# Performance work log

Hardware: AMD Instinct MI355X
Metric: run time of the kernel (lower is better)

The kernel has to match this reference:

```python
import jax, jax.numpy as jnp
import numpy as np

N_NODES = 50000
N_EDGES = 800000
DIMS = [100, 512, 256, 128, 200]  # input -> conv1 -> conv2 -> conv3 -> conv4


def setup_inputs() -> dict:
    key = jax.random.key(0)
    ks = jax.random.split(key, 2 + 4)
    x = jax.random.normal(ks[0], (N_NODES, DIMS[0]), dtype=jnp.float32)
    edge_index = jax.random.randint(ks[1], (2, N_EDGES), 0, N_NODES, dtype=jnp.int64)
    inp = {"x": x, "edge_index": edge_index}
    for i in range(4):
        fan_in = DIMS[i]
        W = jax.random.normal(ks[2 + i], (DIMS[i], DIMS[i + 1]), dtype=jnp.float32) * (1.0 / np.sqrt(fan_in)).astype(np.float32)
        b = jnp.zeros((DIMS[i + 1],), dtype=jnp.float32)
        inp[f"W{i + 1}"] = W
        inp[f"b{i + 1}"] = b
    return inp


def _gcn_layer(x, row, col, norm, W, b, n):
    # PyG GCNConv: linear transform first, then normalized scatter-add, then bias.
    h = x @ W                           # [N, out]
    msg = h[row] * norm[:, None]        # [E+N, out] gather + edge scale
    agg = jax.ops.segment_sum(msg, col, num_segments=n)  # scatter-add to targets
    return agg + b


def reference(x, edge_index, W1, b1, W2, b2, W3, b3, W4, b4):
    n = x.shape[0]
    loop = jnp.arange(n, dtype=edge_index.dtype)
    row = jnp.concatenate([edge_index[0], loop])  # sources (with self-loops)
    col = jnp.concatenate([edge_index[1], loop])  # targets (with self-loops)
    deg = jax.ops.segment_sum(jnp.ones_like(col, dtype=x.dtype), col, num_segments=n)
    dinv = jnp.where(deg > 0, jax.lax.rsqrt(deg), 0.0)
    norm = dinv[row] * dinv[col]  # symmetric D^{-1/2}(A+I)D^{-1/2} edge weights

    out = jax.nn.relu(_gcn_layer(x, row, col, norm, W1, b1, n))
    out = jax.nn.relu(_gcn_layer(out, row, col, norm, W2, b2, n))
    out = jax.nn.relu(_gcn_layer(out, row, col, norm, W3, b3, n))
    out = jax.nn.relu(_gcn_layer(out, row, col, norm, W4, b4, n))
    return jnp.mean(out, axis=0, keepdims=True)  # [1, 200]
```

## Files before the change

### kernel.cpp

```cpp
#include <hip/hip_runtime.h>
#include <hip/hip_bf16.h>


#define NN 50000
#define NE 800000
#define PRANGE (NN / 8)
#define CAP 64

typedef __attribute__((ext_vector_type(8))) _Float16 f16x8;
typedef __attribute__((ext_vector_type(4))) float floatx4;
typedef __attribute__((ext_vector_type(2))) float floatx2;

union U16x8 {
    uint4 u4;
    f16x8 h;
    _Float16 e[8];
};

__device__ __forceinline__ void dec16(const unsigned char* p, float* f) {
    uint4 v = *(const uint4*)p;
    unsigned w[4] = {v.x, v.y, v.z, v.w};
#pragma unroll
    for (int k = 0; k < 4; k++) {
        floatx2 lo = __builtin_amdgcn_cvt_pk_f32_fp8(w[k], false);
        floatx2 hi = __builtin_amdgcn_cvt_pk_f32_fp8(w[k], true);
        f[k * 4 + 0] = lo[0];
        f[k * 4 + 1] = lo[1];
        f[k * 4 + 2] = hi[0];
        f[k * 4 + 3] = hi[1];
    }
}

__device__ __forceinline__ uint4 enc16(const float* f) {
    uint4 r;
    unsigned w;
    w = __builtin_amdgcn_cvt_pk_fp8_f32(f[0], f[1], 0, false);
    w = __builtin_amdgcn_cvt_pk_fp8_f32(f[2], f[3], (int)w, true);
    r.x = w;
    w = __builtin_amdgcn_cvt_pk_fp8_f32(f[4], f[5], 0, false);
    w = __builtin_amdgcn_cvt_pk_fp8_f32(f[6], f[7], (int)w, true);
    r.y = w;
    w = __builtin_amdgcn_cvt_pk_fp8_f32(f[8], f[9], 0, false);
    w = __builtin_amdgcn_cvt_pk_fp8_f32(f[10], f[11], (int)w, true);
    r.z = w;
    w = __builtin_amdgcn_cvt_pk_fp8_f32(f[12], f[13], 0, false);
    w = __builtin_amdgcn_cvt_pk_fp8_f32(f[14], f[15], (int)w, true);
    r.w = w;
    return r;
}

__device__ __forceinline__ uint4 dec8_f16(uint2 v) {
    floatx2 f0 = __builtin_amdgcn_cvt_pk_f32_fp8(v.x, false);
    floatx2 f1 = __builtin_amdgcn_cvt_pk_f32_fp8(v.x, true);
    floatx2 f2 = __builtin_amdgcn_cvt_pk_f32_fp8(v.y, false);
    floatx2 f3 = __builtin_amdgcn_cvt_pk_f32_fp8(v.y, true);
    U16x8 o;
    o.e[0] = (_Float16)f0[0]; o.e[1] = (_Float16)f0[1];
    o.e[2] = (_Float16)f1[0]; o.e[3] = (_Float16)f1[1];
    o.e[4] = (_Float16)f2[0]; o.e[5] = (_Float16)f2[1];
    o.e[6] = (_Float16)f3[0]; o.e[7] = (_Float16)f3[1];
    return o.u4;
}

__global__ __launch_bounds__(256) void zero_kernel(unsigned* __restrict__ fillc,
                                                   float* __restrict__ out) {
    int tid = blockIdx.x * 256 + threadIdx.x;
    if (tid < NN) fillc[tid] = 0u;
    if (blockIdx.x == 0 && threadIdx.x < 200) out[threadIdx.x] = 0.f;
}

__global__ __launch_bounds__(256) void fillcast_kernel(
    const void* __restrict__ ei, unsigned* __restrict__ fillc,
    int* __restrict__ ep, const float* __restrict__ x,
    unsigned char* __restrict__ xb,
    const float* __restrict__ W1, const float* __restrict__ W2,
    const float* __restrict__ W3, const float* __restrict__ W4,
    _Float16* __restrict__ w1t, _Float16* __restrict__ w2t,
    _Float16* __restrict__ w3t, _Float16* __restrict__ w4t) {
    int bx = blockIdx.x, t = threadIdx.x;
    if (bx < 6256) {
        const int part = bx & 7;
        const int lo = part * PRANGE, hi = lo + PRANGE;
        const int group = bx >> 3;
        const int base = (group * 256 + t) * 4;
        __shared__ int nz;
        if (t == 0) nz = 0;
        __syncthreads();
        int dbase = (base <= NE - 4) ? base : (NE - 4);
        unsigned w = ((const unsigned*)ei)[2 * (size_t)dbase + 1];
        if (w) atomicOr(&nz, 1);
        __syncthreads();
        const int f64 = (nz == 0);
        const long long* p64 = (const long long*)ei;
        const int* p32 = (const int*)ei;
#pragma unroll
        for (int i = 0; i < 4; i++) {
            int e = base + i;
            if (e >= NE) break;
            int c = f64 ? (int)p64[NE + e] : p32[NE + e];
            if (c >= lo && c < hi) {
                int idx = (int)atomicAdd(&fillc[c], 1u);
                if (idx < CAP) {
                    int r = f64 ? (int)p64[e] : p32[e];
                    ep[c * CAP + idx] = r;
                }
            }
        }
        return;
    }
    if (bx < 6256 + 1563) {
        int tid = (bx - 6256) * 256 + t;
        int node = tid >> 3, sub = tid & 7;
        if (node >= NN) return;
        int base = sub * 16;
        float f[16];
#pragma unroll
        for (int i = 0; i < 16; i++) {
            int cc = base + i;
            f[i] = (cc < 100) ? x[(size_t)node * 100 + cc] : 0.f;
        }
        *(uint4*)(xb + (size_t)node * 128 + base) = enc16(f);
        return;
    }
    int b = bx - 6256 - 1563;
    const float* W;
    _Float16* Wt;
    int K, N, Kpad, tid;
    if (b < 256)      { W = W1; Wt = w1t; K = 100; N = 512; Kpad = 128; tid = b * 256 + t; }
    else if (b < 768) { W = W2; Wt = w2t; K = 512; N = 256; Kpad = 512; tid = (b - 256) * 256 + t; }
    else if (b < 896) { W = W3; Wt = w3t; K = 256; N = 128; Kpad = 256; tid = (b - 768) * 256 + t; }
    else              { W = W4; Wt = w4t; K = 128; N = 200; Kpad = 128; tid = (b - 896) * 256 + t; }
    int n = tid / Kpad, k = tid - n * Kpad;
    float v = (k < K && n < N) ? W[(size_t)k * N + n] : 0.f;
    Wt[tid] = (_Float16)v;
}

template <int D, int BR, int PS, int SS>
__global__ __launch_bounds__(256) void agg_kernel(
    const unsigned char* __restrict__ H, const int* __restrict__ ep,
    const unsigned* __restrict__ fillc, const float* __restrict__ bias,
    unsigned char* __restrict__ O) {
    constexpr int LPN = D / 16;
    int tid = blockIdx.x * 256 + threadIdx.x;
    int node = tid / LPN;
    int sub = tid % LPN;
    if (node >= NN) return;
    int degt = (int)fillc[node];
    int deg = degt > CAP ? CAP : degt;
    const int s = node * CAP;
    const int e = s + deg;
    float dc = rsqrtf((float)(degt + 1));
    const int base = sub * 16;
    const unsigned char* __restrict__ Hb = H + base;
    float acc[16], t0[16], t1[16];
    dec16(Hb + (size_t)node * D, t0);
    if (SS) {
#pragma unroll
        for (int i = 0; i < 16; i++) acc[i] = t0[i];
        int j = s;
        for (; j + 2 <= e; j += 2) {
            int r0 = ep[j];
            int r1 = ep[j + 1];
            dec16(Hb + (size_t)r0 * D, t0);
            dec16(Hb + (size_t)r1 * D, t1);
#pragma unroll
            for (int i = 0; i < 16; i++) acc[i] += t0[i];
#pragma unroll
            for (int i = 0; i < 16; i++) acc[i] += t1[i];
        }
        if (j < e) {
            int r0 = ep[j];
            dec16(Hb + (size_t)r0 * D, t0);
#pragma unroll
            for (int i = 0; i < 16; i++) acc[i] += t0[i];
        }
#pragma unroll
        for (int i = 0; i < 16; i++) acc[i] *= dc;
    } else {
        float selfw = dc * dc;
#pragma unroll
        for (int i = 0; i < 16; i++) acc[i] = selfw * t0[i];
        int j = s;
        for (; j + 2 <= e; j += 2) {
            int r0 = ep[j];
            int r1 = ep[j + 1];
            float w0 = rsqrtf((float)((int)fillc[r0] + 1)) * dc;
            float w1 = rsqrtf((float)((int)fillc[r1] + 1)) * dc;
            dec16(Hb + (size_t)r0 * D, t0);
            dec16(Hb + (size_t)r1 * D, t1);
#pragma unroll
            for (int i = 0; i < 16; i++) acc[i] = fmaf(w0, t0[i], acc[i]);
#pragma unroll
            for (int i = 0; i < 16; i++) acc[i] = fmaf(w1, t1[i], acc[i]);
        }
        if (j < e) {
            int r0 = ep[j];
            float w0 = rsqrtf((float)((int)fillc[r0] + 1)) * dc;
            dec16(Hb + (size_t)r0 * D, t0);
#pragma unroll
            for (int i = 0; i < 16; i++) acc[i] = fmaf(w0, t0[i], acc[i]);
        }
    }
    if (BR) {
#pragma unroll
        for (int i = 0; i < 16; i++) acc[i] = fmaxf(acc[i] + bias[base + i], 0.f);
    }
    if (PS) {
#pragma unroll
        for (int i = 0; i < 16; i++) acc[i] *= dc;
    }
    *(uint4*)(O + (size_t)node * D + base) = enc16(acc);
}

template <int EPI, int PS>
__global__ __launch_bounds__(256) void gemm_kernel(
    const unsigned char* __restrict__ A, const _Float16* __restrict__ B,
    const float* __restrict__ bias, const unsigned* __restrict__ fillc,
    unsigned char* __restrict__ Cb, float* __restrict__ outmean,
    int M, int K, int N) {
    __shared__ _Float16 Asl[128 * 36];
    __shared__ _Float16 Bsl[128 * 36];
    __shared__ float red[128];
    const int m0 = blockIdx.y * 128;
    const int n0 = blockIdx.x * 128;
    const int t = threadIdx.x;
    const int lane = t & 63, w = t >> 6;
    const int wm = (w >> 1) * 64, wn = (w & 1) * 64;
    const int r16 = lane & 15, quad = lane >> 4;

    const int arow = t >> 1, ac16 = (t & 1) * 16;
    int gma = m0 + arow; if (gma > M - 1) gma = M - 1;
    const unsigned char* Aptr = A + (size_t)gma * K + ac16;
    const int rb0 = t >> 2, kb0 = (t & 3) * 8;
    const int rb1 = (t + 256) >> 2, kb1 = kb0;
    const _Float16* Bptr0 = B + (size_t)(n0 + rb0) * K + kb0;
    const _Float16* Bptr1 = B + (size_t)(n0 + rb1) * K + kb1;

    floatx4 acc[4][4];
    const floatx4 fz = {0.f, 0.f, 0.f, 0.f};
#pragma unroll
    for (int i = 0; i < 4; i++)
#pragma unroll
        for (int j = 0; j < 4; j++) acc[i][j] = fz;

    uint4 apf = *(const uint4*)Aptr;
    uint4 bpf0 = *(const uint4*)Bptr0;
    uint4 bpf1 = *(const uint4*)Bptr1;

    for (int kc = 0; kc < K; kc += 32) {
        __syncthreads();
        uint2 alo = {apf.x, apf.y}, ahi = {apf.z, apf.w};
        *(uint4*)(Asl + arow * 36 + ac16) = dec8_f16(alo);
        *(uint4*)(Asl + arow * 36 + ac16 + 8) = dec8_f16(ahi);
        *(uint4*)(Bsl + rb0 * 36 + kb0) = bpf0;
        *(uint4*)(Bsl + rb1 * 36 + kb1) = bpf1;
        __syncthreads();
        if (kc + 32 < K) {
            apf = *(const uint4*)(Aptr + kc + 32);
            bpf0 = *(const uint4*)(Bptr0 + kc + 32);
            bpf1 = *(const uint4*)(Bptr1 + kc + 32);
        }
        f16x8 af[4], bf[4];
#pragma unroll
        for (int i = 0; i < 4; i++)
            af[i] = *(const f16x8*)(Asl + (wm + i * 16 + r16) * 36 + quad * 8);
#pragma unroll
        for (int j = 0; j < 4; j++)
            bf[j] = *(const f16x8*)(Bsl + (wn + j * 16 + r16) * 36 + quad * 8);
#pragma unroll
        for (int i = 0; i < 4; i++)
#pragma unroll
            for (int j = 0; j < 4; j++)
                acc[i][j] = __builtin_amdgcn_mfma_f32_16x16x32_f16(af[i], bf[j], acc[i][j], 0, 0, 0);
    }

    if (EPI == 2) {
        if (t < 128) red[t] = 0.f;
        __syncthreads();
#pragma unroll
        for (int j = 0; j < 4; j++) {
            int col = n0 + wn + j * 16 + r16;
            float s = 0.f;
            if (col < N) {
                float bv = bias[col];
#pragma unroll
                for (int i = 0; i < 4; i++) {
                    int mbase = m0 + wm + i * 16 + quad * 4;
#pragma unroll
                    for (int r = 0; r < 4; r++)
                        if (mbase + r < M) s += fmaxf(acc[i][j][r] + bv, 0.f);
                }
            }
            atomicAdd(&red[wn + j * 16 + r16], s);
        }
        __syncthreads();
        if (t < 128) {
            int col = n0 + t;
            if (col < N) atomicAdd(outmean + col, red[t] * (1.0f / (float)NN));
        }
    } else {
#pragma unroll
        for (int i = 0; i < 4; i++) {
            int mbase = m0 + wm + i * 16 + quad * 4;
#pragma unroll
            for (int r = 0; r < 4; r++) {
                int m = mbase + r;
                if (m >= M) continue;
                float dsc = 1.f;
                if (PS) dsc = rsqrtf((float)((int)fillc[m] + 1));
#pragma unroll
                for (int j = 0; j < 4; j++) {
                    int col = n0 + wn + j * 16 + r16;
                    float v = acc[i][j][r];
                    if (EPI == 1) v = fmaxf(v + bias[col], 0.f);
                    if (PS) v *= dsc;
                    unsigned pk = __builtin_amdgcn_cvt_pk_fp8_f32(v, v, 0, false);
                    Cb[(size_t)m * N + col] = (unsigned char)(pk & 0xffu);
                }
            }
        }
    }
}

extern "C" void kernel_launch(void* const* d_in, const int* in_sizes, int n_in,
                              void* d_out, int out_size, void* d_ws, size_t ws_size,
                              hipStream_t stream) {
    const float* x  = (const float*)d_in[0];
    const void*  ei = d_in[1];
    const float* W1 = (const float*)d_in[2];
    const float* b1 = (const float*)d_in[3];
    const float* W2 = (const float*)d_in[4];
    const float* b2 = (const float*)d_in[5];
    const float* W3 = (const float*)d_in[6];
    const float* b3 = (const float*)d_in[7];
    const float* W4 = (const float*)d_in[8];
    const float* b4 = (const float*)d_in[9];
    float* out = (float*)d_out;

    char* ws = (char*)d_ws;
    size_t o = 0;
    auto alloc = [&](size_t bytes) -> void* {
        void* p = ws + o;
        o += (bytes + 255) & ~(size_t)255;
        return p;
    };
    unsigned* fillc = (unsigned*)alloc((size_t)NN * 4);
    int*      ep    = (int*)alloc((size_t)NN * CAP * 4);
    _Float16* w1t = (_Float16*)alloc((size_t)512 * 128 * 2);
    _Float16* w2t = (_Float16*)alloc((size_t)256 * 512 * 2);
    _Float16* w3t = (_Float16*)alloc((size_t)128 * 256 * 2);
    _Float16* w4t = (_Float16*)alloc((size_t)256 * 128 * 2);
    unsigned char* xb  = (unsigned char*)alloc((size_t)NN * 128);
    unsigned char* A1b = (unsigned char*)alloc((size_t)NN * 128);
    unsigned char* H1b = (unsigned char*)alloc((size_t)NN * 512);
    unsigned char* t2b = (unsigned char*)alloc((size_t)NN * 256);
    unsigned char* H2b = (unsigned char*)alloc((size_t)NN * 256);
    unsigned char* t3b = (unsigned char*)alloc((size_t)NN * 128);
    unsigned char* h3b = (unsigned char*)alloc((size_t)NN * 128);
    unsigned char* A4b = (unsigned char*)alloc((size_t)NN * 128);

    zero_kernel<<<196, 256, 0, stream>>>(fillc, out);
    fillcast_kernel<<<6256 + 1563 + 1024, 256, 0, stream>>>(
        ei, fillc, ep, x, xb, W1, W2, W3, W4, w1t, w2t, w3t, w4t);

    const int MB128 = (NN + 127) / 128;
    const int AB128 = (NN * 8 + 255) / 256;
    const int AB256 = (NN * 16 + 255) / 256;

    agg_kernel<128, 0, 0, 0><<<AB128, 256, 0, stream>>>(xb, ep, fillc, nullptr, A1b);
    gemm_kernel<1, 0><<<dim3(4, MB128), 256, 0, stream>>>(A1b, w1t, b1, fillc, H1b, nullptr, NN, 128, 512);
    gemm_kernel<0, 1><<<dim3(2, MB128), 256, 0, stream>>>(H1b, w2t, nullptr, fillc, t2b, nullptr, NN, 512, 256);
    agg_kernel<256, 1, 0, 1><<<AB256, 256, 0, stream>>>(t2b, ep, fillc, b2, H2b);
    gemm_kernel<0, 1><<<dim3(1, MB128), 256, 0, stream>>>(H2b, w3t, nullptr, fillc, t3b, nullptr, NN, 256, 128);
    agg_kernel<128, 1, 1, 1><<<AB128, 256, 0, stream>>>(t3b, ep, fillc, b3, h3b);
    agg_kernel<128, 0, 0, 1><<<AB128, 256, 0, stream>>>(h3b, ep, fillc, nullptr, A4b);
    gemm_kernel<2, 0><<<dim3(2, MB128), 256, 0, stream>>>(A4b, w4t, b4, fillc, nullptr, out, NN, 128, 200);
}
```

Baseline: 307.4 us.

## Build CSR adjacency via two-pass partitioned bucketing with LDS counters

Replaces the edge-bucketing pass, which ran 8 partition passes over all edges with global atomics per target node, with two stages. First, edges are binned into 25 partition queues of 2048 nodes each, using block-local LDS counts and one global atomic per partition per block. Second, one block per partition scatters its queue into the per-node adjacency lists with LDS atomics and then writes the fill counts. This cuts global atomic traffic and repeated reads of the edge list. In exchange it adds a kernel launch and packs (col<<16|row) into 32 bits, so row indices above 65535 would be truncated. With only 25 blocks doing the scatter, that stage has limited parallelism, and each queue silently drops edges past its 65536 capacity.

```diff
diff --git a/kernel.cpp b/kernel.cpp
--- a/kernel.cpp
+++ b/kernel.cpp
@@ -4,8 +4,10 @@
 
 #define NN 50000
 #define NE 800000
-#define PRANGE (NN / 8)
 #define CAP 64
+#define NPART 25
+#define QCAP 65536
+#define P1B 1563
 
 typedef __attribute__((ext_vector_type(8))) _Float16 f16x8;
 typedef __attribute__((ext_vector_type(4))) float floatx4;
@@ -62,54 +64,93 @@
     return o.u4;
 }
 
-__global__ __launch_bounds__(256) void zero_kernel(unsigned* __restrict__ fillc,
+__global__ __launch_bounds__(256) void zero_kernel(unsigned* __restrict__ qtail,
                                                    float* __restrict__ out) {
-    int tid = blockIdx.x * 256 + threadIdx.x;
-    if (tid < NN) fillc[tid] = 0u;
-    if (blockIdx.x == 0 && threadIdx.x < 200) out[threadIdx.x] = 0.f;
-}
-
-__global__ __launch_bounds__(256) void fillcast_kernel(
-    const void* __restrict__ ei, unsigned* __restrict__ fillc,
-    int* __restrict__ ep, const float* __restrict__ x,
-    unsigned char* __restrict__ xb,
+    int t = threadIdx.x;
+    if (t < NPART) qtail[t] = 0u;
+    if (t < 200) out[t] = 0.f;
+}
+
+__global__ __launch_bounds__(256) void p1_kernel(const void* __restrict__ ei,
+                                                 unsigned* __restrict__ q,
+                                                 unsigned* __restrict__ qtail) {
+    __shared__ int nz;
+    __shared__ unsigned cnt[NPART], gbase[NPART], cur[NPART];
+    int bx = blockIdx.x, t = threadIdx.x;
+    const int base = (bx * 256 + t) * 2;
+    if (t < NPART) { cnt[t] = 0u; cur[t] = 0u; }
+    if (t == 0) nz = 0;
+    __syncthreads();
+    int eb = (base <= NE - 2) ? base : (NE - 2);
+    unsigned w = ((const unsigned*)ei)[2 * (size_t)eb + 1];
+    if (w) atomicOr(&nz, 1);
+    __syncthreads();
+    const int f64 = (nz == 0);
+    const long long* p64 = (const long long*)ei;
+    const int* p32 = (const int*)ei;
+    int c0 = 0, c1 = 0, r0 = 0, r1 = 0;
+    const bool valid = (base < NE);
+    if (valid) {
+        if (f64) {
+            c0 = (int)p64[NE + base];
+            c1 = (int)p64[NE + base + 1];
+            r0 = (int)p64[base];
+            r1 = (int)p64[base + 1];
+        } else {
+            c0 = p32[NE + base];
+            c1 = p32[NE + base + 1];
+            r0 = p32[base];
+            r1 = p32[base + 1];
+        }
+        atomicAdd(&cnt[c0 >> 11], 1u);
+        atomicAdd(&cnt[c1 >> 11], 1u);
+    }
+    __syncthreads();
+    if (t < NPART && cnt[t]) gbase[t] = atomicAdd(&qtail[t], cnt[t]);
+    __syncthreads();
+    if (valid) {
+        unsigned p0 = (unsigned)c0 >> 11, p1 = (unsigned)c1 >> 11;
+        unsigned l0 = atomicAdd(&cur[p0], 1u);
+        unsigned o0 = gbase[p0] + l0;
+        if (o0 < QCAP) q[p0 * QCAP + o0] = ((unsigned)c0 << 16) | (unsigned)r0;
+        unsigned l1 = atomicAdd(&cur[p1], 1u);
+        unsigned o1 = gbase[p1] + l1;
+        if (o1 < QCAP) q[p1 * QCAP + o1] = ((unsigned)c1 << 16) | (unsigned)r1;
+    }
+}
+
+__global__ __launch_bounds__(256) void fill2cast_kernel(
+    const unsigned* __restrict__ q, const unsigned* __restrict__ qtail,
+    unsigned* __restrict__ fillc, int* __restrict__ ep,
+    const float* __restrict__ x, unsigned char* __restrict__ xb,
     const float* __restrict__ W1, const float* __restrict__ W2,
     const float* __restrict__ W3, const float* __restrict__ W4,
     _Float16* __restrict__ w1t, _Float16* __restrict__ w2t,
     _Float16* __restrict__ w3t, _Float16* __restrict__ w4t) {
     int bx = blockIdx.x, t = threadIdx.x;
-    if (bx < 6256) {
-        const int part = bx & 7;
-        const int lo = part * PRANGE, hi = lo + PRANGE;
-        const int group = bx >> 3;
-        const int base = (group * 256 + t) * 4;
-        __shared__ int nz;
-        if (t == 0) nz = 0;
-        __syncthreads();
-        int dbase = (base <= NE - 4) ? base : (NE - 4);
-        unsigned w = ((const unsigned*)ei)[2 * (size_t)dbase + 1];
-        if (w) atomicOr(&nz, 1);
-        __syncthreads();
-        const int f64 = (nz == 0);
-        const long long* p64 = (const long long*)ei;
-        const int* p32 = (const int*)ei;
-#pragma unroll
-        for (int i = 0; i < 4; i++) {
-            int e = base + i;
-            if (e >= NE) break;
-            int c = f64 ? (int)p64[NE + e] : p32[NE + e];
-            if (c >= lo && c < hi) {
-                int idx = (int)atomicAdd(&fillc[c], 1u);
-                if (idx < CAP) {
-                    int r = f64 ? (int)p64[e] : p32[e];
-                    ep[c * CAP + idx] = r;
-                }
-            }
-        }
+    if (bx < NPART) {
+        __shared__ unsigned cnt[2048];
+        const int n0 = bx << 11;
+        for (int i = t; i < 2048; i += 256) cnt[i] = 0u;
+        __syncthreads();
+        unsigned qlen = qtail[bx];
+        if (qlen > QCAP) qlen = QCAP;
+        const unsigned* qp = q + (size_t)bx * QCAP;
+        for (unsigned i = t; i < qlen; i += 256) {
+            unsigned e = qp[i];
+            int c = (int)(e >> 16);
+            int r = (int)(e & 0xffffu);
+            unsigned idx = atomicAdd(&cnt[c - n0], 1u);
+            if (idx < CAP) ep[c * CAP + idx] = r;
+        }
+        __syncthreads();
+        int nn = NN - n0;
+        if (nn > 2048) nn = 2048;
+        for (int i = t; i < nn; i += 256) fillc[n0 + i] = cnt[i];
         return;
     }
-    if (bx < 6256 + 1563) {
-        int tid = (bx - 6256) * 256 + t;
+    if (bx < NPART + 1563) {
+        int tid = (bx - NPART) * 256 + t;
         int node = tid >> 3, sub = tid & 7;
         if (node >= NN) return;
         int base = sub * 16;
@@ -122,7 +163,7 @@
         *(uint4*)(xb + (size_t)node * 128 + base) = enc16(f);
         return;
     }
-    int b = bx - 6256 - 1563;
+    int b = bx - NPART - 1563;
     const float* W;
     _Float16* Wt;
     int K, N, Kpad, tid;
@@ -346,6 +387,8 @@
     };
     unsigned* fillc = (unsigned*)alloc((size_t)NN * 4);
     int*      ep    = (int*)alloc((size_t)NN * CAP * 4);
+    unsigned* q     = (unsigned*)alloc((size_t)NPART * QCAP * 4);
+    unsigned* qtail = (unsigned*)alloc((size_t)NPART * 4);
     _Float16* w1t = (_Float16*)alloc((size_t)512 * 128 * 2);
     _Float16* w2t = (_Float16*)alloc((size_t)256 * 512 * 2);
     _Float16* w3t = (_Float16*)alloc((size_t)128 * 256 * 2);
@@ -359,9 +402,10 @@
     unsigned char* h3b = (unsigned char*)alloc((size_t)NN * 128);
     unsigned char* A4b = (unsigned char*)alloc((size_t)NN * 128);
 
-    zero_kernel<<<196, 256, 0, stream>>>(fillc, out);
-    fillcast_kernel<<<6256 + 1563 + 1024, 256, 0, stream>>>(
-        ei, fillc, ep, x, xb, W1, W2, W3, W4, w1t, w2t, w3t, w4t);
+    zero_kernel<<<1, 256, 0, stream>>>(qtail, out);
+    p1_kernel<<<P1B, 256, 0, stream>>>(ei, q, qtail);
+    fill2cast_kernel<<<NPART + 1563 + 1024, 256, 0, stream>>>(
+        q, qtail, fillc, ep, x, xb, W1, W2, W3, W4, w1t, w2t, w3t, w4t);
 
     const int MB128 = (NN + 127) / 128;
     const int AB128 = (NN * 8 + 255) / 256;
```

Result: slower. 341.0 us (+11.0%).

## Split aggregation features into 64-column slabs for cache-resident gathers

Applied to the files above, without the earlier changes.

Feature matrices feeding the aggregation steps are now stored in column slabs of 64 bytes per node (NN*64 each), written that way by the cast kernel and by the GEMM epilogue. Each aggregation runs as several launches, one per slab, so the randomly gathered working set per launch is 3.2 MB and should stay in L2/MALL instead of thrashing. Outputs use nontemporal stores. The cost is extra kernel launches, the edge list being re-read once per slab, and scattered byte stores in the GEMM epilogue.

```diff
diff --git a/kernel.cpp b/kernel.cpp
--- a/kernel.cpp
+++ b/kernel.cpp
@@ -10,6 +10,7 @@
 typedef __attribute__((ext_vector_type(8))) _Float16 f16x8;
 typedef __attribute__((ext_vector_type(4))) float floatx4;
 typedef __attribute__((ext_vector_type(2))) float floatx2;
+typedef __attribute__((ext_vector_type(4))) unsigned uintx4;
 
 union U16x8 {
     uint4 u4;
@@ -49,6 +50,12 @@
     return r;
 }
 
+__device__ __forceinline__ void nt_store16(unsigned char* p, uint4 v) {
+    union { uint4 a; uintx4 b; } u;
+    u.a = v;
+    __builtin_nontemporal_store(u.b, (uintx4*)p);
+}
+
 __device__ __forceinline__ uint4 dec8_f16(uint2 v) {
     floatx2 f0 = __builtin_amdgcn_cvt_pk_f32_fp8(v.x, false);
     floatx2 f1 = __builtin_amdgcn_cvt_pk_f32_fp8(v.x, true);
@@ -119,7 +126,8 @@
             int cc = base + i;
             f[i] = (cc < 100) ? x[(size_t)node * 100 + cc] : 0.f;
         }
-        *(uint4*)(xb + (size_t)node * 128 + base) = enc16(f);
+        *(uint4*)(xb + (size_t)(sub >> 2) * ((size_t)NN * 64) +
+                  (size_t)node * 64 + (sub & 3) * 16) = enc16(f);
         return;
     }
     int b = bx - 6256 - 1563;
@@ -135,15 +143,14 @@
     Wt[tid] = (_Float16)v;
 }
 
-template <int D, int BR, int PS, int SS>
-__global__ __launch_bounds__(256) void agg_kernel(
-    const unsigned char* __restrict__ H, const int* __restrict__ ep,
-    const unsigned* __restrict__ fillc, const float* __restrict__ bias,
-    unsigned char* __restrict__ O) {
-    constexpr int LPN = D / 16;
+template <int BR, int PS, int SS>
+__global__ __launch_bounds__(256) void agg64_kernel(
+    const unsigned char* __restrict__ Hs, const int* __restrict__ ep,
+    const unsigned* __restrict__ fillc, const float* __restrict__ biasp,
+    unsigned char* __restrict__ Op, int ostride) {
     int tid = blockIdx.x * 256 + threadIdx.x;
-    int node = tid / LPN;
-    int sub = tid % LPN;
+    int node = tid >> 2;
+    int sub = tid & 3;
     if (node >= NN) return;
     int degt = (int)fillc[node];
     int deg = degt > CAP ? CAP : degt;
@@ -151,9 +158,9 @@
     const int e = s + deg;
     float dc = rsqrtf((float)(degt + 1));
     const int base = sub * 16;
-    const unsigned char* __restrict__ Hb = H + base;
+    const unsigned char* __restrict__ Hb = Hs + base;
     float acc[16], t0[16], t1[16];
-    dec16(Hb + (size_t)node * D, t0);
+    dec16(Hb + (size_t)node * 64, t0);
     if (SS) {
 #pragma unroll
         for (int i = 0; i < 16; i++) acc[i] = t0[i];
@@ -161,8 +168,8 @@
         for (; j + 2 <= e; j += 2) {
             int r0 = ep[j];
             int r1 = ep[j + 1];
-            dec16(Hb + (size_t)r0 * D, t0);
-            dec16(Hb + (size_t)r1 * D, t1);
+            dec16(Hb + (size_t)r0 * 64, t0);
+            dec16(Hb + (size_t)r1 * 64, t1);
 #pragma unroll
             for (int i = 0; i < 16; i++) acc[i] += t0[i];
 #pragma unroll
@@ -170,7 +177,7 @@
         }
         if (j < e) {
             int r0 = ep[j];
-            dec16(Hb + (size_t)r0 * D, t0);
+            dec16(Hb + (size_t)r0 * 64, t0);
 #pragma unroll
             for (int i = 0; i < 16; i++) acc[i] += t0[i];
         }
@@ -186,8 +193,8 @@
             int r1 = ep[j + 1];
             float w0 = rsqrtf((float)((int)fillc[r0] + 1)) * dc;
             float w1 = rsqrtf((float)((int)fillc[r1] + 1)) * dc;
-            dec16(Hb + (size_t)r0 * D, t0);
-            dec16(Hb + (size_t)r1 * D, t1);
+            dec16(Hb + (size_t)r0 * 64, t0);
+            dec16(Hb + (size_t)r1 * 64, t1);
 #pragma unroll
             for (int i = 0; i < 16; i++) acc[i] = fmaf(w0, t0[i], acc[i]);
 #pragma unroll
@@ -196,23 +203,23 @@
         if (j < e) {
             int r0 = ep[j];
             float w0 = rsqrtf((float)((int)fillc[r0] + 1)) * dc;
-            dec16(Hb + (size_t)r0 * D, t0);
+            dec16(Hb + (size_t)r0 * 64, t0);
 #pragma unroll
             for (int i = 0; i < 16; i++) acc[i] = fmaf(w0, t0[i], acc[i]);
         }
     }
     if (BR) {
 #pragma unroll
-        for (int i = 0; i < 16; i++) acc[i] = fmaxf(acc[i] + bias[base + i], 0.f);
+        for (int i = 0; i < 16; i++) acc[i] = fmaxf(acc[i] + biasp[base + i], 0.f);
     }
     if (PS) {
 #pragma unroll
         for (int i = 0; i < 16; i++) acc[i] *= dc;
     }
-    *(uint4*)(O + (size_t)node * D + base) = enc16(acc);
-}
-
-template <int EPI, int PS>
+    nt_store16(Op + (size_t)node * ostride + base, enc16(acc));
+}
+
+template <int EPI, int PS, int OBLK>
 __global__ __launch_bounds__(256) void gemm_kernel(
     const unsigned char* __restrict__ A, const _Float16* __restrict__ B,
     const float* __restrict__ bias, const unsigned* __restrict__ fillc,
@@ -315,7 +322,11 @@
                     if (EPI == 1) v = fmaxf(v + bias[col], 0.f);
                     if (PS) v *= dsc;
                     unsigned pk = __builtin_amdgcn_cvt_pk_fp8_f32(v, v, 0, false);
-                    Cb[(size_t)m * N + col] = (unsigned char)(pk & 0xffu);
+                    if (OBLK)
+                        Cb[(size_t)(col >> 6) * ((size_t)NN * 64) +
+                           (size_t)m * 64 + (col & 63)] = (unsigned char)(pk & 0xffu);
+                    else
+                        Cb[(size_t)m * N + col] = (unsigned char)(pk & 0xffu);
                 }
             }
         }
@@ -364,15 +375,21 @@
         ei, fillc, ep, x, xb, W1, W2, W3, W4, w1t, w2t, w3t, w4t);
 
     const int MB128 = (NN + 127) / 128;
-    const int AB128 = (NN * 8 + 255) / 256;
-    const int AB256 = (NN * 16 + 255) / 256;
-
-    agg_kernel<128, 0, 0, 0><<<AB128, 256, 0, stream>>>(xb, ep, fillc, nullptr, A1b);
-    gemm_kernel<1, 0><<<dim3(4, MB128), 256, 0, stream>>>(A1b, w1t, b1, fillc, H1b, nullptr, NN, 128, 512);
-    gemm_kernel<0, 1><<<dim3(2, MB128), 256, 0, stream>>>(H1b, w2t, nullptr, fillc, t2b, nullptr, NN, 512, 256);
-    agg_kernel<256, 1, 0, 1><<<AB256, 256, 0, stream>>>(t2b, ep, fillc, b2, H2b);
-    gemm_kernel<0, 1><<<dim3(1, MB128), 256, 0, stream>>>(H2b, w3t, nullptr, fillc, t3b, nullptr, NN, 256, 128);
-    agg_kernel<128, 1, 1, 1><<<AB128, 256, 0, stream>>>(t3b, ep, fillc, b3, h3b);
-    agg_kernel<128, 0, 0, 1><<<AB128, 256, 0, stream>>>(h3b, ep, fillc, nullptr, A4b);
-    gemm_kernel<2, 0><<<dim3(2, MB128), 256, 0, stream>>>(A4b, w4t, b4, fillc, nullptr, out, NN, 128, 200);
-}
+    const int AGB = (NN * 4 + 255) / 256;
+    const size_t SLAB = (size_t)NN * 64;
+
+    agg64_kernel<0, 0, 0><<<AGB, 256, 0, stream>>>(xb,        ep, fillc, nullptr, A1b,      128);
+    agg64_kernel<0, 0, 0><<<AGB, 256, 0, stream>>>(xb + SLAB, ep, fillc, nullptr, A1b + 64, 128);
+    gemm_kernel<1, 0, 0><<<dim3(4, MB128), 256, 0, stream>>>(A1b, w1t, b1, fillc, H1b, nullptr, NN, 128, 512);
+    gemm_kernel<0, 1, 1><<<dim3(2, MB128), 256, 0, stream>>>(H1b, w2t, nullptr, fillc, t2b, nullptr, NN, 512, 256);
+    agg64_kernel<1, 0, 1><<<AGB, 256, 0, stream>>>(t2b,            ep, fillc, b2,       H2b,       256);
+    agg64_kernel<1, 0, 1><<<AGB, 256, 0, stream>>>(t2b + SLAB,     ep, fillc, b2 + 64,  H2b + 64,  256);
+    agg64_kernel<1, 0, 1><<<AGB, 256, 0, stream>>>(t2b + 2 * SLAB, ep, fillc, b2 + 128, H2b + 128, 256);
+    agg64_kernel<1, 0, 1><<<AGB, 256, 0, stream>>>(t2b + 3 * SLAB, ep, fillc, b2 + 192, H2b + 192, 256);
+    gemm_kernel<0, 1, 1><<<dim3(1, MB128), 256, 0, stream>>>(H2b, w3t, nullptr, fillc, t3b, nullptr, NN, 256, 128);
+    agg64_kernel<1, 1, 1><<<AGB, 256, 0, stream>>>(t3b,        ep, fillc, b3,      h3b,        64);
+    agg64_kernel<1, 1, 1><<<AGB, 256, 0, stream>>>(t3b + SLAB, ep, fillc, b3 + 64, h3b + SLAB, 64);
+    agg64_kernel<0, 0, 1><<<AGB, 256, 0, stream>>>(h3b,        ep, fillc, nullptr, A4b,      128);
+    agg64_kernel<0, 0, 1><<<AGB, 256, 0, stream>>>(h3b + SLAB, ep, fillc, nullptr, A4b + 64, 128);
+    gemm_kernel<2, 0, 0><<<dim3(2, MB128), 256, 0, stream>>>(A4b, w4t, b4, fillc, nullptr, out, NN, 128, 200);
+}
```

After: 370.3 us. +20.5%, slower.

## Fuse neighbor aggregation into following GEMM for layers one and four

Applied to the files above, without the earlier changes.

Adds a fused kernel that gathers and normalizes neighbor rows for a 64-node tile directly into shared memory as fp16, then runs MFMA against the weight tiles over all output columns. It replaces the separate aggregation and GEMM launches for layer 1 and layer 4, removing the fp8 round-trip of the aggregated intermediate through global memory and two launches. The cost is smaller M tiles (64 rows) and more sequential N-tiles per block. For layer 1 that means four passes over 512 columns, which may reduce GEMM efficiency and parallelism.

```diff
diff --git a/kernel.cpp b/kernel.cpp
--- a/kernel.cpp
+++ b/kernel.cpp
@@ -212,6 +212,179 @@
     *(uint4*)(O + (size_t)node * D + base) = enc16(acc);
 }
 
+template <int SS, int EPI>
+__global__ __launch_bounds__(256) void aggemm_kernel(
+    const unsigned char* __restrict__ H, const int* __restrict__ ep,
+    const unsigned* __restrict__ fillc, const float* __restrict__ bias,
+    const _Float16* __restrict__ B, unsigned char* __restrict__ Cb,
+    float* __restrict__ outmean, int N) {
+    __shared__ _Float16 Alds[4][64][36];
+    __shared__ _Float16 Bsl[128 * 36];
+    __shared__ float red[128];
+    const int m0 = blockIdx.x * 64;
+    const int t = threadIdx.x;
+
+#pragma unroll
+    for (int it = 0; it < 2; ++it) {
+        int u = t + it * 256;
+        int nl = u >> 3;
+        int sub = u & 7;
+        int node = m0 + nl;
+        int nd = node < NN ? node : NN - 1;
+        int degt = (int)fillc[nd];
+        int deg = degt > CAP ? CAP : degt;
+        const int s = nd * CAP;
+        const int e = s + deg;
+        float dc = rsqrtf((float)(degt + 1));
+        const int base = sub * 16;
+        const unsigned char* __restrict__ Hb = H + base;
+        float acc[16], t0[16], t1[16];
+        dec16(Hb + (size_t)nd * 128, t0);
+        if (SS) {
+#pragma unroll
+            for (int i = 0; i < 16; i++) acc[i] = t0[i];
+            int j = s;
+            for (; j + 2 <= e; j += 2) {
+                int r0 = ep[j];
+                int r1 = ep[j + 1];
+                dec16(Hb + (size_t)r0 * 128, t0);
+                dec16(Hb + (size_t)r1 * 128, t1);
+#pragma unroll
+                for (int i = 0; i < 16; i++) acc[i] += t0[i];
+#pragma unroll
+                for (int i = 0; i < 16; i++) acc[i] += t1[i];
+            }
+            if (j < e) {
+                int r0 = ep[j];
+                dec16(Hb + (size_t)r0 * 128, t0);
+#pragma unroll
+                for (int i = 0; i < 16; i++) acc[i] += t0[i];
+            }
+#pragma unroll
+            for (int i = 0; i < 16; i++) acc[i] *= dc;
+        } else {
+            float selfw = dc * dc;
+#pragma unroll
+            for (int i = 0; i < 16; i++) acc[i] = selfw * t0[i];
+            int j = s;
+            for (; j + 2 <= e; j += 2) {
+                int r0 = ep[j];
+                int r1 = ep[j + 1];
+                float w0 = rsqrtf((float)((int)fillc[r0] + 1)) * dc;
+                float w1 = rsqrtf((float)((int)fillc[r1] + 1)) * dc;
+                dec16(Hb + (size_t)r0 * 128, t0);
+                dec16(Hb + (size_t)r1 * 128, t1);
+#pragma unroll
+                for (int i = 0; i < 16; i++) acc[i] = fmaf(w0, t0[i], acc[i]);
+#pragma unroll
+                for (int i = 0; i < 16; i++) acc[i] = fmaf(w1, t1[i], acc[i]);
+            }
+            if (j < e) {
+                int r0 = ep[j];
+                float w0 = rsqrtf((float)((int)fillc[r0] + 1)) * dc;
+                dec16(Hb + (size_t)r0 * 128, t0);
+#pragma unroll
+                for (int i = 0; i < 16; i++) acc[i] = fmaf(w0, t0[i], acc[i]);
+            }
+        }
+        U16x8 lo, hi;
+#pragma unroll
+        for (int i = 0; i < 8; i++) { lo.e[i] = (_Float16)acc[i]; hi.e[i] = (_Float16)acc[8 + i]; }
+        _Float16* dst = &Alds[sub >> 1][nl][(sub & 1) * 16];
+        *(uint4*)dst = lo.u4;
+        *(uint4*)(dst + 8) = hi.u4;
+    }
+    __syncthreads();
+
+    const int lane = t & 63, w = t >> 6;
+    const int wm = (w >> 1) * 32, wn = (w & 1) * 64;
+    const int r16 = lane & 15, quad = lane >> 4;
+    const int rb0 = t >> 2, kb0 = (t & 3) * 8;
+    const int rb1 = (t + 256) >> 2;
+    const int NT = (N + 127) / 128;
+
+    for (int nt = 0; nt < NT; ++nt) {
+        const int n0 = nt * 128;
+        const _Float16* Bp0 = B + (size_t)(n0 + rb0) * 128 + kb0;
+        const _Float16* Bp1 = B + (size_t)(n0 + rb1) * 128 + kb0;
+        floatx4 acc[2][4];
+        const floatx4 fz = {0.f, 0.f, 0.f, 0.f};
+#pragma unroll
+        for (int i = 0; i < 2; i++)
+#pragma unroll
+            for (int j = 0; j < 4; j++) acc[i][j] = fz;
+        uint4 bpf0 = *(const uint4*)Bp0;
+        uint4 bpf1 = *(const uint4*)Bp1;
+#pragma unroll
+        for (int kc = 0; kc < 128; kc += 32) {
+            __syncthreads();
+            *(uint4*)(Bsl + rb0 * 36 + kb0) = bpf0;
+            *(uint4*)(Bsl + rb1 * 36 + kb0) = bpf1;
+            __syncthreads();
+            if (kc + 32 < 128) {
+                bpf0 = *(const uint4*)(Bp0 + kc + 32);
+                bpf1 = *(const uint4*)(Bp1 + kc + 32);
+            }
+            f16x8 af[2], bf[4];
+#pragma unroll
+            for (int i = 0; i < 2; i++)
+                af[i] = *(const f16x8*)(&Alds[kc >> 5][wm + i * 16 + r16][quad * 8]);
+#pragma unroll
+            for (int j = 0; j < 4; j++)
+                bf[j] = *(const f16x8*)(Bsl + (wn + j * 16 + r16) * 36 + quad * 8);
+#pragma unroll
+            for (int i = 0; i < 2; i++)
+#pragma unroll
+                for (int j = 0; j < 4; j++)
+                    acc[i][j] = __builtin_amdgcn_mfma_f32_16x16x32_f16(af[i], bf[j], acc[i][j], 0, 0, 0);
+        }
+        if (EPI == 2) {
+            __syncthreads();
+            if (t < 128) red[t] = 0.f;
+            __syncthreads();
+#pragma unroll
+            for (int j = 0; j < 4; j++) {
+                int col = n0 + wn + j * 16 + r16;
+                float s = 0.f;
+                if (col < N) {
+                    float bv = bias[col];
+#pragma unroll
+                    for (int i = 0; i < 2; i++) {
+                        int mbase = m0 + wm + i * 16 + quad * 4;
+#pragma unroll
+                        for (int r = 0; r < 4; r++)
+                            if (mbase + r < NN) s += fmaxf(acc[i][j][r] + bv, 0.f);
+                    }
+                }
+                atomicAdd(&red[wn + j * 16 + r16], s);
+            }
+            __syncthreads();
+            if (t < 128) {
+                int col = n0 + t;
+                if (col < N) atomicAdd(outmean + col, red[t] * (1.0f / (float)NN));
+            }
+        } else {
+#pragma unroll
+            for (int i = 0; i < 2; i++) {
+                int mbase = m0 + wm + i * 16 + quad * 4;
+#pragma unroll
+                for (int r = 0; r < 4; r++) {
+                    int m = mbase + r;
+                    if (m >= NN) continue;
+#pragma unroll
+                    for (int j = 0; j < 4; j++) {
+                        int col = n0 + wn + j * 16 + r16;
+                        float v = acc[i][j][r];
+                        v = fmaxf(v + bias[col], 0.f);
+                        unsigned pk = __builtin_amdgcn_cvt_pk_fp8_f32(v, v, 0, false);
+                        Cb[(size_t)m * N + col] = (unsigned char)(pk & 0xffu);
+                    }
+                }
+            }
+        }
+    }
+}
+
 template <int EPI, int PS>
 __global__ __launch_bounds__(256) void gemm_kernel(
     const unsigned char* __restrict__ A, const _Float16* __restrict__ B,
@@ -220,7 +393,6 @@
     int M, int K, int N) {
     __shared__ _Float16 Asl[128 * 36];
     __shared__ _Float16 Bsl[128 * 36];
-    __shared__ float red[128];
     const int m0 = blockIdx.y * 128;
     const int n0 = blockIdx.x * 128;
     const int t = threadIdx.x;
@@ -232,9 +404,9 @@
     int gma = m0 + arow; if (gma > M - 1) gma = M - 1;
     const unsigned char* Aptr = A + (size_t)gma * K + ac16;
     const int rb0 = t >> 2, kb0 = (t & 3) * 8;
-    const int rb1 = (t + 256) >> 2, kb1 = kb0;
+    const int rb1 = (t + 256) >> 2;
     const _Float16* Bptr0 = B + (size_t)(n0 + rb0) * K + kb0;
-    const _Float16* Bptr1 = B + (size_t)(n0 + rb1) * K + kb1;
+    const _Float16* Bptr1 = B + (size_t)(n0 + rb1) * K + kb0;
 
     floatx4 acc[4][4];
     const floatx4 fz = {0.f, 0.f, 0.f, 0.f};
@@ -253,7 +425,7 @@
         *(uint4*)(Asl + arow * 36 + ac16) = dec8_f16(alo);
         *(uint4*)(Asl + arow * 36 + ac16 + 8) = dec8_f16(ahi);
         *(uint4*)(Bsl + rb0 * 36 + kb0) = bpf0;
-        *(uint4*)(Bsl + rb1 * 36 + kb1) = bpf1;
+        *(uint4*)(Bsl + rb1 * 36 + kb0) = bpf1;
         __syncthreads();
         if (kc + 32 < K) {
             apf = *(const uint4*)(Aptr + kc + 32);
@@ -274,49 +446,23 @@
                 acc[i][j] = __builtin_amdgcn_mfma_f32_16x16x32_f16(af[i], bf[j], acc[i][j], 0, 0, 0);
     }
 
-    if (EPI == 2) {
-        if (t < 128) red[t] = 0.f;
-        __syncthreads();
-#pragma unroll
-        for (int j = 0; j < 4; j++) {
-            int col = n0 + wn + j * 16 + r16;
-            float s = 0.f;
-            if (col < N) {
-                float bv = bias[col];
-#pragma unroll
-                for (int i = 0; i < 4; i++) {
-                    int mbase = m0 + wm + i * 16 + quad * 4;
-#pragma unroll
-                    for (int r = 0; r < 4; r++)
-                        if (mbase + r < M) s += fmaxf(acc[i][j][r] + bv, 0.f);
-                }
-            }
-            atomicAdd(&red[wn + j * 16 + r16], s);
-        }
-        __syncthreads();
-        if (t < 128) {
-            int col = n0 + t;
-            if (col < N) atomicAdd(outmean + col, red[t] * (1.0f / (float)NN));
-        }
-    } else {
-#pragma unroll
-        for (int i = 0; i < 4; i++) {
-            int mbase = m0 + wm + i * 16 + quad * 4;
-#pragma unroll
-            for (int r = 0; r < 4; r++) {
-                int m = mbase + r;
-                if (m >= M) continue;
-                float dsc = 1.f;
-                if (PS) dsc = rsqrtf((float)((int)fillc[m] + 1));
-#pragma unroll
-                for (int j = 0; j < 4; j++) {
-                    int col = n0 + wn + j * 16 + r16;
-                    float v = acc[i][j][r];
-                    if (EPI == 1) v = fmaxf(v + bias[col], 0.f);
-                    if (PS) v *= dsc;
-                    unsigned pk = __builtin_amdgcn_cvt_pk_fp8_f32(v, v, 0, false);
-                    Cb[(size_t)m * N + col] = (unsigned char)(pk & 0xffu);
-                }
+#pragma unroll
+    for (int i = 0; i < 4; i++) {
+        int mbase = m0 + wm + i * 16 + quad * 4;
+#pragma unroll
+        for (int r = 0; r < 4; r++) {
+            int m = mbase + r;
+            if (m >= M) continue;
+            float dsc = 1.f;
+            if (PS) dsc = rsqrtf((float)((int)fillc[m] + 1));
+#pragma unroll
+            for (int j = 0; j < 4; j++) {
+                int col = n0 + wn + j * 16 + r16;
+                float v = acc[i][j][r];
+                if (EPI == 1) v = fmaxf(v + bias[col], 0.f);
+                if (PS) v *= dsc;
+                unsigned pk = __builtin_amdgcn_cvt_pk_fp8_f32(v, v, 0, false);
+                Cb[(size_t)m * N + col] = (unsigned char)(pk & 0xffu);
             }
         }
     }
@@ -351,28 +497,25 @@
     _Float16* w3t = (_Float16*)alloc((size_t)128 * 256 * 2);
     _Float16* w4t = (_Float16*)alloc((size_t)256 * 128 * 2);
     unsigned char* xb  = (unsigned char*)alloc((size_t)NN * 128);
-    unsigned char* A1b = (unsigned char*)alloc((size_t)NN * 128);
     unsigned char* H1b = (unsigned char*)alloc((size_t)NN * 512);
     unsigned char* t2b = (unsigned char*)alloc((size_t)NN * 256);
     unsigned char* H2b = (unsigned char*)alloc((size_t)NN * 256);
     unsigned char* t3b = (unsigned char*)alloc((size_t)NN * 128);
     unsigned char* h3b = (unsigned char*)alloc((size_t)NN * 128);
-    unsigned char* A4b = (unsigned char*)alloc((size_t)NN * 128);
 
     zero_kernel<<<196, 256, 0, stream>>>(fillc, out);
     fillcast_kernel<<<6256 + 1563 + 1024, 256, 0, stream>>>(
         ei, fillc, ep, x, xb, W1, W2, W3, W4, w1t, w2t, w3t, w4t);
 
+    const int MB64 = (NN + 63) / 64;
     const int MB128 = (NN + 127) / 128;
     const int AB128 = (NN * 8 + 255) / 256;
     const int AB256 = (NN * 16 + 255) / 256;
 
-    agg_kernel<128, 0, 0, 0><<<AB128, 256, 0, stream>>>(xb, ep, fillc, nullptr, A1b);
-    gemm_kernel<1, 0><<<dim3(4, MB128), 256, 0, stream>>>(A1b, w1t, b1, fillc, H1b, nullptr, NN, 128, 512);
+    aggemm_kernel<0, 1><<<MB64, 256, 0, stream>>>(xb, ep, fillc, b1, w1t, H1b, nullptr, 512);
     gemm_kernel<0, 1><<<dim3(2, MB128), 256, 0, stream>>>(H1b, w2t, nullptr, fillc, t2b, nullptr, NN, 512, 256);
     agg_kernel<256, 1, 0, 1><<<AB256, 256, 0, stream>>>(t2b, ep, fillc, b2, H2b);
     gemm_kernel<0, 1><<<dim3(1, MB128), 256, 0, stream>>>(H2b, w3t, nullptr, fillc, t3b, nullptr, NN, 256, 128);
     agg_kernel<128, 1, 1, 1><<<AB128, 256, 0, stream>>>(t3b, ep, fillc, b3, h3b);
-    agg_kernel<128, 0, 0, 1><<<AB128, 256, 0, stream>>>(h3b, ep, fillc, nullptr, A4b);
-    gemm_kernel<2, 0><<<dim3(2, MB128), 256, 0, stream>>>(A4b, w4t, b4, fillc, nullptr, out, NN, 128, 200);
-}
+    aggemm_kernel<1, 2><<<MB64, 256, 0, stream>>>(h3b, ep, fillc, b4, w4t, nullptr, out, 200);
+}
```

New measurement: 320.3 us. 1.04x slower.
